# Performance work log

Hardware: AMD Instinct MI355X
Metric: run time of the kernel (lower is better)

The kernel has to match this reference:

```python
import jax, jax.numpy as jnp
import numpy as np
from jax import lax

B, C, H, W = 8, 384, 64, 64


def cos_map(N):
    # ortho DCT-II basis: weight[n, x] = cos(n*(x+0.5)*pi/N) * sqrt(2/N), row 0 /= sqrt(2)
    wx = (jnp.arange(N, dtype=jnp.float32) + 0.5) / N
    wn = jnp.arange(N, dtype=jnp.float32)[:, None]
    w = jnp.cos(wn * wx[None, :] * jnp.pi) * np.sqrt(2.0 / N).astype(np.float32)
    return w.at[0, :].multiply(np.float32(1.0 / np.sqrt(2.0)))


def setup_inputs() -> dict:
    key = jax.random.key(0)
    ks = jax.random.split(key, 8)
    s = 0.05
    return {
        "x": jax.random.normal(ks[0], (B, C, H, W), jnp.float32),
        "freq_embed": jax.random.normal(ks[1], (H, W, C), jnp.float32),
        "dw_w": jax.random.normal(ks[2], (C, 1, 3, 3), jnp.float32) * s,
        "dw_b": jnp.zeros((C,), jnp.float32),
        "lin_w": jax.random.normal(ks[3], (2 * C, C), jnp.float32) * s,
        "lin_b": jnp.zeros((2 * C,), jnp.float32),
        "tok_w": jax.random.normal(ks[4], (C, C), jnp.float32) * s,
        "tok_b": jnp.zeros((C,), jnp.float32),
        "c": jnp.ones((1,), jnp.float32),
        "alpha": jnp.ones((1,), jnp.float32) * 0.1,
        "ln_g": jnp.ones((C,), jnp.float32),
        "ln_b": jnp.zeros((C,), jnp.float32),
        "out_w": jax.random.normal(ks[5], (C, C), jnp.float32) * s,
        "out_b": jnp.zeros((C,), jnp.float32),
    }


def reference(x, freq_embed, dw_w, dw_b, lin_w, lin_b, tok_w, tok_b, c, alpha, ln_g, ln_b, out_w, out_b):
    Bc, Cc, Hc, Wc = x.shape
    # depthwise 3x3 conv
    x = lax.conv_general_dilated(x, dw_w, (1, 1), 'SAME',
                                 feature_group_count=Cc,
                                 dimension_numbers=('NCHW', 'OIHW', 'NCHW'))
    x = x + dw_b[None, :, None, None]
    # linear to 2C (channels-last), split into signal x and gate z
    xz = jnp.einsum('bchw,dc->bhwd', x, lin_w) + lin_b
    xs, z = xz[..., :Cc], xz[..., Cc:]          # [B,H,W,C]
    xs = jnp.transpose(xs, (0, 3, 1, 2))        # [B,C,H,W]
    # 2D ortho DCT-II: D = Wh @ x @ Ww^T
    Wh, Ww = cos_map(Hc), cos_map(Wc)
    Xd = jnp.einsum('nh,bchw,kw->bcnk', Wh, xs, Ww)
    # learned frequency gating: t = ReLU(Linear(freq_embed)), per (H,W,C)
    t = jax.nn.relu(jnp.einsum('hwc,dc->hwd', freq_embed, tok_w) + tok_b)
    ct = jnp.transpose(jnp.cos(c * t), (2, 0, 1))[None]        # [1,C,H,W]
    st = jnp.transpose(jnp.sin(c * t), (2, 0, 1))[None] / c[0]
    # x_u0 == x_v0 == Xd in the original (dct2d applied twice to same x)
    final = ct * Xd + st * (Xd + 0.5 * alpha[0] * Xd)
    # 2D inverse DCT: x = Wh^T @ D @ Ww
    xi = jnp.einsum('nh,bcnk,kw->bchw', Wh, final, Ww)
    # LayerNorm over channels, gate with SiLU(z), output linear
    y = jnp.transpose(xi, (0, 2, 3, 1))          # [B,H,W,C]
    mu = jnp.mean(y, axis=-1, keepdims=True)
    var = jnp.mean((y - mu) ** 2, axis=-1, keepdims=True)
    y = (y - mu) * lax.rsqrt(var + 1e-5) * ln_g + ln_b
    y = y * jax.nn.silu(z)
    y = jnp.einsum('bhwc,dc->bhwd', y, out_w) + out_b
    return jnp.transpose(y, (0, 3, 1, 2))        # [B,C,H,W]
```

## Files before the change

### kernel.cpp

```cpp
#include <hip/hip_runtime.h>

typedef _Float16 h2 __attribute__((ext_vector_type(2)));
typedef _Float16 h4 __attribute__((ext_vector_type(4)));
typedef _Float16 h8 __attribute__((ext_vector_type(8)));
typedef float    f4 __attribute__((ext_vector_type(4)));

#define MFMA32(a,b,c) __builtin_amdgcn_mfma_f32_16x16x32_f16((a),(b),(c),0,0,0)
#define MFMA16(a,b,c) __builtin_amdgcn_mfma_f32_16x16x16f16((a),(b),(c),0,0,0)

#define B_N 8
#define C_N 384
#define P_N 4096
#define PI_F 3.14159265358979323846f

__device__ __forceinline__ h4 to_h4(f4 v) {
  h4 r; r[0]=(_Float16)v[0]; r[1]=(_Float16)v[1]; r[2]=(_Float16)v[2]; r[3]=(_Float16)v[3];
  return r;
}

__device__ __forceinline__ void gl_lds16(const _Float16* g, _Float16* l) {
  __builtin_amdgcn_global_load_lds(
      (const __attribute__((address_space(1))) void*)g,
      (__attribute__((address_space(3))) void*)l, 16, 0, 0);
}

__global__ __launch_bounds__(256) void k_setup(
    const float* __restrict__ lin_w, const float* __restrict__ tok_w,
    const float* __restrict__ out_w, _Float16* __restrict__ lwh,
    _Float16* __restrict__ twh, _Float16* __restrict__ owh,
    _Float16* __restrict__ wmg, _Float16* __restrict__ wmtg) {
  int t = blockIdx.x * 256 + threadIdx.x;
  if (t < 768*384) lwh[t] = (_Float16)lin_w[t];
  if (t < 384*384) { twh[t] = (_Float16)tok_w[t]; owh[t] = (_Float16)out_w[t]; }
  if (t < 4096) {
    int n = t >> 6, h = t & 63;
    float v = cosf((float)n * ((float)h + 0.5f) * (PI_F / 64.0f)) * 0.1767766952966369f;
    if (n == 0) v *= 0.7071067811865476f;
    wmg[n*64 + h]  = (_Float16)v;
    wmtg[h*64 + n] = (_Float16)v;
  }
}

__global__ __launch_bounds__(256) void k_dwconv(
    const float* __restrict__ x, const float* __restrict__ dww,
    const float* __restrict__ dwb, _Float16* __restrict__ xdw) {
  int blk = blockIdx.x;
  int h = blk & 63;
  int rest = blk >> 6;
  int cgi = rest % 6;
  int b = rest / 6;
  int c0 = cgi * 64;
  int t = threadIdx.x;
  int w = t & 63, ci = t >> 6;
  __shared__ _Float16 buf[64 * 68];
  const float* xb = x + (size_t)b * C_N * P_N;
  int wl = (w > 0)  ? w - 1 : 0;
  int wr = (w < 63) ? w + 1 : 63;
  #pragma unroll
  for (int j = 0; j < 8; j++) {
    int lc = ci * 16 + j * 2;
    h2 pr;
    #pragma unroll
    for (int e = 0; e < 2; e++) {
      int c = c0 + lc + e;
      const float* xc = xb + (size_t)c * P_N;
      float k0=dww[c*9+0],k1=dww[c*9+1],k2=dww[c*9+2];
      float k3=dww[c*9+3],k4=dww[c*9+4],k5=dww[c*9+5];
      float k6=dww[c*9+6],k7=dww[c*9+7],k8=dww[c*9+8];
      float top = (h > 0)  ? xc[(h-1)*64 + w] : 0.0f;
      float mid = xc[h*64 + w];
      float bot = (h < 63) ? xc[(h+1)*64 + w] : 0.0f;
      float tl = __shfl(top, wl, 64), tr = __shfl(top, wr, 64);
      float ml = __shfl(mid, wl, 64), mr = __shfl(mid, wr, 64);
      float bl = __shfl(bot, wl, 64), br = __shfl(bot, wr, 64);
      if (w == 0)  { tl = 0.f; ml = 0.f; bl = 0.f; }
      if (w == 63) { tr = 0.f; mr = 0.f; br = 0.f; }
      float acc = dwb[c];
      acc += k0*tl + k1*top + k2*tr;
      acc += k3*ml + k4*mid + k5*mr;
      acc += k6*bl + k7*bot + k8*br;
      pr[e] = (_Float16)acc;
    }
    *(h2*)&buf[w*68 + lc] = pr;
  }
  __syncthreads();
  _Float16* op = xdw + ((size_t)b*P_N + h*64) * C_N + c0;
  #pragma unroll
  for (int i = 0; i < 4; i++) {
    int flat = (t + 256*i) * 4;
    int pix = flat >> 6, cl = flat & 63;
    *(h4*)&op[(size_t)pix*C_N + cl] = *(const h4*)&buf[pix*68 + cl];
  }
}

__global__ __launch_bounds__(256) void k_gate(
    const float* __restrict__ fe, const _Float16* __restrict__ twh,
    const float* __restrict__ tkb, const float* __restrict__ cc,
    const float* __restrict__ aa, _Float16* __restrict__ g) {
  int pt = blockIdx.x & 63, dt = blockIdx.x >> 6;
  int p0 = pt*64, d0 = dt*64;
  int t = threadIdx.x, lane = t & 63, wave = t >> 6;
  int quad = lane >> 4, l15 = lane & 15;
  int wm_ = wave >> 1, wn = wave & 1;
  __shared__ _Float16 la[64*40], lb[64*40];
  int srow = t >> 2, scg = (t & 3) * 8;
  f4 acc[2][2] = {};
  for (int kc = 0; kc < 384; kc += 32) {
    const float* src = fe + (size_t)(p0 + srow)*384 + kc + scg;
    f4 v0 = *(const f4*)src;
    f4 v1 = *(const f4*)(src + 4);
    h8 hv;
    hv[0]=(_Float16)v0[0]; hv[1]=(_Float16)v0[1]; hv[2]=(_Float16)v0[2]; hv[3]=(_Float16)v0[3];
    hv[4]=(_Float16)v1[0]; hv[5]=(_Float16)v1[1]; hv[6]=(_Float16)v1[2]; hv[7]=(_Float16)v1[3];
    *(h8*)&la[srow*40 + scg] = hv;
    *(h8*)&lb[srow*40 + scg] = *(const h8*)&twh[(size_t)(d0 + srow)*384 + kc + scg];
    __syncthreads();
    h8 a0 = *(const h8*)&la[(wm_*32 + l15)*40 + quad*8];
    h8 a1 = *(const h8*)&la[(wm_*32 + 16 + l15)*40 + quad*8];
    h8 b0 = *(const h8*)&lb[(wn*32 + l15)*40 + quad*8];
    h8 b1 = *(const h8*)&lb[(wn*32 + 16 + l15)*40 + quad*8];
    acc[0][0] = MFMA32(a0, b0, acc[0][0]);
    acc[0][1] = MFMA32(a0, b1, acc[0][1]);
    acc[1][0] = MFMA32(a1, b0, acc[1][0]);
    acc[1][1] = MFMA32(a1, b1, acc[1][1]);
    __syncthreads();
  }
  float c0 = cc[0];
  float s1 = (1.0f + 0.5f*aa[0]) / c0;
  #pragma unroll
  for (int i = 0; i < 2; i++)
  #pragma unroll
  for (int j = 0; j < 2; j++) {
    int d  = d0 + wn*32 + j*16 + l15;
    int pl = wm_*32 + i*16 + quad*4;
    float bias = tkb[d];
    h4 hv;
    #pragma unroll
    for (int r = 0; r < 4; r++) {
      float tv = fmaxf(acc[i][j][r] + bias, 0.0f);
      hv[r] = (_Float16)(__cosf(c0*tv) + s1*__sinf(c0*tv));
    }
    *(h4*)&g[(size_t)d*P_N + p0 + pl] = hv;
  }
}

__global__ __launch_bounds__(256) void k_gemm1(
    const _Float16* __restrict__ xdw, const _Float16* __restrict__ lwh,
    const float* __restrict__ lnb, _Float16* __restrict__ xs,
    _Float16* __restrict__ zs) {
  int pt = blockIdx.x & 31;
  int rest = blockIdx.x >> 5;
  int dt = rest % 6, b = rest / 6;
  int p0 = pt * 128, d0 = dt * 128;
  int t = threadIdx.x, lane = t & 63, wave = t >> 6;
  int quad = lane >> 4, l15 = lane & 15;
  int wm = wave >> 1, wn = wave & 1;
  __shared__ _Float16 la[128 * 32];
  __shared__ _Float16 lb[128 * 32];
  int s_row = lane >> 2;
  int s_col = (lane & 3) * 8;
  const _Float16* ga = xdw + ((size_t)b*P_N + p0) * 384 + s_col;
  const _Float16* gb = lwh + (size_t)d0 * 384 + s_col;
  f4 acc[4][4] = {};
  for (int kc = 0; kc < 384; kc += 32) {
    #pragma unroll
    for (int s = 0; s < 2; s++) {
      int seg = wave * 2 + s;
      int row = seg * 16 + s_row;
      gl_lds16(ga + (size_t)row*384 + kc, &la[seg*512 + lane*8]);
      gl_lds16(gb + (size_t)row*384 + kc, &lb[seg*512 + lane*8]);
    }
    __syncthreads();
    h8 af[4], bf[4];
    #pragma unroll
    for (int i = 0; i < 4; i++) {
      af[i] = *(const h8*)&la[(wm*64 + i*16 + l15)*32 + quad*8];
      bf[i] = *(const h8*)&lb[(wn*64 + i*16 + l15)*32 + quad*8];
    }
    #pragma unroll
    for (int i = 0; i < 4; i++)
    #pragma unroll
    for (int j = 0; j < 4; j++)
      acc[i][j] = MFMA32(af[i], bf[j], acc[i][j]);
    __syncthreads();
  }
  bool isz = (d0 >= 384);
  #pragma unroll
  for (int j = 0; j < 4; j++) {
    int d = d0 + wn*64 + j*16 + l15;
    float bias = lnb[d];
    _Float16* dst = isz ? (zs + ((size_t)b*C_N + (d-384)) * P_N)
                        : (xs + ((size_t)b*C_N + d) * P_N);
    #pragma unroll
    for (int i = 0; i < 4; i++) {
      int p = p0 + wm*64 + i*16 + quad*4;
      h4 hv;
      if (isz) {
        #pragma unroll
        for (int r = 0; r < 4; r++) {
          float v = acc[i][j][r] + bias;
          v = v / (1.0f + __expf(-v));
          hv[r] = (_Float16)v;
        }
      } else {
        #pragma unroll
        for (int r = 0; r < 4; r++) hv[r] = (_Float16)(acc[i][j][r] + bias);
      }
      *(h4*)&dst[p] = hv;
    }
  }
}

__global__ __launch_bounds__(256) void k_dct(
    const _Float16* __restrict__ xs, const _Float16* __restrict__ g,
    const _Float16* __restrict__ wmg, const _Float16* __restrict__ wmtg,
    _Float16* __restrict__ xi) {
  int b = blockIdx.x / 96, cg = blockIdx.x % 96;
  int c0 = cg * 4;
  int t = threadIdx.x, wave = t >> 6, lane = t & 63;
  int quad = lane >> 4, l15 = lane & 15;
  __shared__ _Float16 wm_s[64*72];
  __shared__ _Float16 wmt_s[64*72];
  __shared__ _Float16 pb[4][64*72];
  for (int i = t; i < 512; i += 256) {
    int row = i >> 3, col = (i & 7) * 8;
    *(h8*)&wm_s[row*72 + col]  = *(const h8*)&wmg[row*64 + col];
    *(h8*)&wmt_s[row*72 + col] = *(const h8*)&wmtg[row*64 + col];
  }
  const _Float16* xsb = xs + ((size_t)b*C_N + c0) * P_N;
  for (int i = t; i < 2048; i += 256) {
    int pl = i >> 9, idx = i & 511;
    int p = idx * 8, hh = p >> 6, ww = p & 63;
    *(h8*)&pb[pl][hh*72 + ww] = *(const h8*)&xsb[(size_t)pl*P_N + p];
  }
  __syncthreads();
  h8 aS[4][2], bW[4][2];
  #pragma unroll
  for (int I = 0; I < 4; I++)
  #pragma unroll
  for (int kk = 0; kk < 2; kk++) {
    aS[I][kk] = *(const h8*)&pb[wave][(I*16 + l15)*72 + kk*32 + quad*8];
    bW[I][kk] = *(const h8*)&wm_s[(I*16 + l15)*72 + kk*32 + quad*8];
  }
  h4 t1h[4][4];
  #pragma unroll
  for (int I = 0; I < 4; I++)
  #pragma unroll
  for (int J = 0; J < 4; J++) {
    f4 a = {};
    a = MFMA32(aS[I][0], bW[J][0], a);
    a = MFMA32(aS[I][1], bW[J][1], a);
    t1h[I][J] = to_h4(a);
  }
  __syncthreads();
  const _Float16* gb = g + (size_t)c0 * P_N;
  for (int i = t; i < 2048; i += 256) {
    int pl = i >> 9, idx = i & 511;
    int p = idx * 8, hh = p >> 6, ww = p & 63;
    *(h8*)&pb[pl][hh*72 + ww] = *(const h8*)&gb[(size_t)pl*P_N + p];
  }
  __syncthreads();
  f4 t2[4][4] = {};
  #pragma unroll
  for (int I = 0; I < 4; I++)
  #pragma unroll
  for (int K4 = 0; K4 < 4; K4++) {
    h4 af = *(const h4*)&wm_s[(I*16 + l15)*72 + K4*16 + quad*4];
    #pragma unroll
    for (int J = 0; J < 4; J++) t2[I][J] = MFMA16(af, t1h[K4][J], t2[I][J]);
  }
  h4 fh[4][4];
  #pragma unroll
  for (int I = 0; I < 4; I++)
  #pragma unroll
  for (int J = 0; J < 4; J++) {
    int n0 = I*16 + quad*4, k = J*16 + l15;
    h4 r;
    #pragma unroll
    for (int rr = 0; rr < 4; rr++) {
      float gv = (float)pb[wave][(n0+rr)*72 + k];
      r[rr] = (_Float16)(t2[I][J][rr] * gv);
    }
    fh[I][J] = r;
  }
  f4 t3[4][4] = {};
  #pragma unroll
  for (int J = 0; J < 4; J++)
  #pragma unroll
  for (int K4 = 0; K4 < 4; K4++) {
    h4 bf = *(const h4*)&wmt_s[(J*16 + l15)*72 + K4*16 + quad*4];
    #pragma unroll
    for (int I = 0; I < 4; I++) t3[I][J] = MFMA16(fh[K4][I], bf, t3[I][J]);
  }
  h4 t3h[4][4];
  #pragma unroll
  for (int I = 0; I < 4; I++)
  #pragma unroll
  for (int J = 0; J < 4; J++) t3h[I][J] = to_h4(t3[I][J]);
  f4 t4[4][4] = {};
  #pragma unroll
  for (int I = 0; I < 4; I++)
  #pragma unroll
  for (int K4 = 0; K4 < 4; K4++) {
    h4 af = *(const h4*)&wmt_s[(I*16 + l15)*72 + K4*16 + quad*4];
    #pragma unroll
    for (int J = 0; J < 4; J++) t4[I][J] = MFMA16(af, t3h[K4][J], t4[I][J]);
  }
  #pragma unroll
  for (int I = 0; I < 4; I++)
  #pragma unroll
  for (int J = 0; J < 4; J++) {
    int w0 = I*16 + quad*4, hq = J*16 + l15;
    *(h4*)&pb[wave][hq*72 + w0] = to_h4(t4[I][J]);
  }
  __syncthreads();
  _Float16* xib = xi + ((size_t)b*C_N + c0) * P_N;
  for (int i = t; i < 2048; i += 256) {
    int pl = i >> 9, idx = i & 511;
    int p = idx * 8, hh = p >> 6, ww = p & 63;
    *(h8*)&xib[(size_t)pl*P_N + p] = *(const h8*)&pb[pl][hh*72 + ww];
  }
}

__global__ __launch_bounds__(256) void k_ubuild(
    const _Float16* __restrict__ xi, const _Float16* __restrict__ zs,
    const float* __restrict__ lng, const float* __restrict__ lnbv,
    _Float16* __restrict__ u) {
  int b = blockIdx.x >> 6, pt = blockIdx.x & 63;
  int p0 = pt * 64;
  int t = threadIdx.x;
  __shared__ _Float16 ut[64 * 392];
  __shared__ float red[4][64], red2[4][64];
  __shared__ float muL[64], rsL[64];
  int cr = t >> 3;
  int px0 = (t & 7) * 8;
  const _Float16* xib = xi + (size_t)b * C_N * P_N;
  #pragma unroll
  for (int i = 0; i < 12; i++) {
    int c = cr + 32 * i;
    h8 v = *(const h8*)&xib[(size_t)c * P_N + p0 + px0];
    #pragma unroll
    for (int e = 0; e < 8; e++) ut[(px0 + e) * 392 + c] = v[e];
  }
  __syncthreads();
  int px = t & 63, seg = t >> 6;
  float s = 0.f, ss = 0.f;
  #pragma unroll
  for (int j = 0; j < 12; j++) {
    h8 v = *(const h8*)&ut[px * 392 + seg * 96 + j * 8];
    #pragma unroll
    for (int e = 0; e < 8; e++) { float f = (float)v[e]; s += f; ss += f * f; }
  }
  red[seg][px] = s; red2[seg][px] = ss;
  __syncthreads();
  if (t < 64) {
    float st  = red[0][t] + red[1][t] + red[2][t] + red[3][t];
    float sst = red2[0][t] + red2[1][t] + red2[2][t] + red2[3][t];
    float m = st * (1.f/384.f);
    float var = sst * (1.f/384.f) - m * m;
    muL[t] = m; rsL[t] = rsqrtf(var + 1e-5f);
  }
  __syncthreads();
  const _Float16* zb = zs + (size_t)b * C_N * P_N;
  #pragma unroll
  for (int i = 0; i < 12; i++) {
    int c = cr + 32 * i;
    float g = lng[c], bb = lnbv[c];
    h8 zv = *(const h8*)&zb[(size_t)c * P_N + p0 + px0];
    #pragma unroll
    for (int e = 0; e < 8; e++) {
      int p = px0 + e;
      float y = ((float)ut[p * 392 + c] - muL[p]) * rsL[p] * g + bb;
      ut[p * 392 + c] = (_Float16)(y * (float)zv[e]);
    }
  }
  __syncthreads();
  _Float16* ub = u + ((size_t)b * P_N + p0) * C_N;
  #pragma unroll
  for (int i = 0; i < 12; i++) {
    int idx = t + 256 * i;
    int row = idx / 48, ch = idx % 48;
    *(h8*)&ub[(size_t)row * C_N + ch * 8] = *(const h8*)&ut[row * 392 + ch * 8];
  }
}

__global__ __launch_bounds__(256) void k_gemm2(
    const _Float16* __restrict__ u, const _Float16* __restrict__ owh,
    const float* __restrict__ ob, float* __restrict__ out) {
  int pt = blockIdx.x & 31;
  int rest = blockIdx.x >> 5;
  int dt = rest % 3, b = rest / 3;
  int p0 = pt * 128, d0 = dt * 128;
  int t = threadIdx.x, lane = t & 63, wave = t >> 6;
  int quad = lane >> 4, l15 = lane & 15;
  int wm = wave >> 1, wn = wave & 1;
  __shared__ _Float16 la[128 * 32];
  __shared__ _Float16 lb[128 * 32];
  int s_row = lane >> 2;
  int s_col = (lane & 3) * 8;
  const _Float16* ga = u   + ((size_t)b*P_N + p0) * 384 + s_col;
  const _Float16* gb = owh + (size_t)d0 * 384 + s_col;
  f4 acc[4][4] = {};
  for (int kc = 0; kc < 384; kc += 32) {
    #pragma unroll
    for (int s = 0; s < 2; s++) {
      int seg = wave * 2 + s;
      int row = seg * 16 + s_row;
      gl_lds16(ga + (size_t)row*384 + kc, &la[seg*512 + lane*8]);
      gl_lds16(gb + (size_t)row*384 + kc, &lb[seg*512 + lane*8]);
    }
    __syncthreads();
    h8 af[4], bf[4];
    #pragma unroll
    for (int i = 0; i < 4; i++) {
      af[i] = *(const h8*)&la[(wm*64 + i*16 + l15)*32 + quad*8];
      bf[i] = *(const h8*)&lb[(wn*64 + i*16 + l15)*32 + quad*8];
    }
    #pragma unroll
    for (int i = 0; i < 4; i++)
    #pragma unroll
    for (int j = 0; j < 4; j++)
      acc[i][j] = MFMA32(af[i], bf[j], acc[i][j]);
    __syncthreads();
  }
  #pragma unroll
  for (int j = 0; j < 4; j++) {
    int d = d0 + wn*64 + j*16 + l15;
    float bias = ob[d];
    #pragma unroll
    for (int i = 0; i < 4; i++) {
      int p = p0 + wm*64 + i*16 + quad*4;
      f4 v;
      #pragma unroll
      for (int r = 0; r < 4; r++) v[r] = acc[i][j][r] + bias;
      *(f4*)&out[((size_t)b*C_N + d)*P_N + p] = v;
    }
  }
}

extern "C" void kernel_launch(void* const* d_in, const int* in_sizes, int n_in,
                              void* d_out, int out_size, void* d_ws, size_t ws_size,
                              hipStream_t stream) {
  (void)in_sizes; (void)n_in; (void)out_size; (void)ws_size;
  const float* x    = (const float*)d_in[0];
  const float* fe   = (const float*)d_in[1];
  const float* dww  = (const float*)d_in[2];
  const float* dwb  = (const float*)d_in[3];
  const float* linw = (const float*)d_in[4];
  const float* linb = (const float*)d_in[5];
  const float* tokw = (const float*)d_in[6];
  const float* tokb = (const float*)d_in[7];
  const float* cc   = (const float*)d_in[8];
  const float* aa   = (const float*)d_in[9];
  const float* lng  = (const float*)d_in[10];
  const float* lnbv = (const float*)d_in[11];
  const float* outw = (const float*)d_in[12];
  const float* outb = (const float*)d_in[13];
  float* out = (float*)d_out;

  char* ws = (char*)d_ws;
  size_t off = 0;
  auto alloc = [&](size_t bytes) -> void* {
    void* p = ws + off;
    off += (bytes + 255) & ~(size_t)255;
    return p;
  };
  _Float16* lwh  = (_Float16*)alloc((size_t)768*384*2);
  _Float16* twh  = (_Float16*)alloc((size_t)384*384*2);
  _Float16* owh  = (_Float16*)alloc((size_t)384*384*2);
  _Float16* wmg  = (_Float16*)alloc((size_t)64*64*2);
  _Float16* wmtg = (_Float16*)alloc((size_t)64*64*2);
  _Float16* xdw  = (_Float16*)alloc((size_t)B_N*P_N*C_N*2);
  _Float16* xs   = (_Float16*)alloc((size_t)B_N*C_N*P_N*2);
  _Float16* zs   = (_Float16*)alloc((size_t)B_N*C_N*P_N*2);
  _Float16* gg   = (_Float16*)alloc((size_t)C_N*P_N*2);
  _Float16* xi   = xdw;
  _Float16* uu   = xs;

  k_setup<<<1152, 256, 0, stream>>>(linw, tokw, outw, lwh, twh, owh, wmg, wmtg);
  k_dwconv<<<3072, 256, 0, stream>>>(x, dww, dwb, xdw);
  k_gate<<<384, 256, 0, stream>>>(fe, twh, tokb, cc, aa, gg);
  k_gemm1<<<1536, 256, 0, stream>>>(xdw, lwh, linb, xs, zs);
  k_dct<<<768, 256, 0, stream>>>(xs, gg, wmg, wmtg, xi);
  k_ubuild<<<512, 256, 0, stream>>>(xi, zs, lng, lnbv, uu);
  k_gemm2<<<768, 256, 0, stream>>>(uu, owh, outb, out);
}
```

Baseline: 257.9 us.

## Stage full-K weight tile in LDS and stream activations from global in GEMMs

Both pointwise GEMMs switch from 128x128 tiles with per-K-step LDS staging of both operands and two barriers per step, to 128x64 tiles. Each block preloads the whole 64x384 weight slice into padded LDS once, and each wave reads its A fragments straight from global memory. This removes the per-iteration barriers and the LDS round-trip for activations, and doubles the grid size. In exchange, each activation row is now read by twice as many blocks, so global A traffic rises, and the direct global loads are not software-pipelined.

```diff
diff --git a/kernel.cpp b/kernel.cpp
--- a/kernel.cpp
+++ b/kernel.cpp
@@ -16,12 +16,6 @@
 __device__ __forceinline__ h4 to_h4(f4 v) {
   h4 r; r[0]=(_Float16)v[0]; r[1]=(_Float16)v[1]; r[2]=(_Float16)v[2]; r[3]=(_Float16)v[3];
   return r;
-}
-
-__device__ __forceinline__ void gl_lds16(const _Float16* g, _Float16* l) {
-  __builtin_amdgcn_global_load_lds(
-      (const __attribute__((address_space(1))) void*)g,
-      (__attribute__((address_space(3))) void*)l, 16, 0, 0);
 }
 
 __global__ __launch_bounds__(256) void k_setup(
@@ -150,50 +144,45 @@
     _Float16* __restrict__ zs) {
   int pt = blockIdx.x & 31;
   int rest = blockIdx.x >> 5;
-  int dt = rest % 6, b = rest / 6;
-  int p0 = pt * 128, d0 = dt * 128;
+  int dt = rest % 12, b = rest / 12;
+  int p0 = pt * 128, d0 = dt * 64;
   int t = threadIdx.x, lane = t & 63, wave = t >> 6;
   int quad = lane >> 4, l15 = lane & 15;
-  int wm = wave >> 1, wn = wave & 1;
-  __shared__ _Float16 la[128 * 32];
-  __shared__ _Float16 lb[128 * 32];
-  int s_row = lane >> 2;
-  int s_col = (lane & 3) * 8;
-  const _Float16* ga = xdw + ((size_t)b*P_N + p0) * 384 + s_col;
-  const _Float16* gb = lwh + (size_t)d0 * 384 + s_col;
-  f4 acc[4][4] = {};
+  __shared__ _Float16 lbs[64 * 392];
+  {
+    int row = t >> 2, cb = (t & 3) * 8;
+    const _Float16* gB = lwh + (size_t)(d0 + row) * 384;
+    #pragma unroll
+    for (int i = 0; i < 12; i++)
+      *(h8*)&lbs[row*392 + cb + i*32] = *(const h8*)&gB[cb + i*32];
+  }
+  __syncthreads();
+  const _Float16* pa = xdw + ((size_t)b*P_N + p0 + wave*32 + l15) * 384 + quad*8;
+  f4 acc[2][4] = {};
+  #pragma unroll
   for (int kc = 0; kc < 384; kc += 32) {
-    #pragma unroll
-    for (int s = 0; s < 2; s++) {
-      int seg = wave * 2 + s;
-      int row = seg * 16 + s_row;
-      gl_lds16(ga + (size_t)row*384 + kc, &la[seg*512 + lane*8]);
-      gl_lds16(gb + (size_t)row*384 + kc, &lb[seg*512 + lane*8]);
-    }
-    __syncthreads();
-    h8 af[4], bf[4];
-    #pragma unroll
-    for (int i = 0; i < 4; i++) {
-      af[i] = *(const h8*)&la[(wm*64 + i*16 + l15)*32 + quad*8];
-      bf[i] = *(const h8*)&lb[(wn*64 + i*16 + l15)*32 + quad*8];
-    }
-    #pragma unroll
-    for (int i = 0; i < 4; i++)
+    h8 a0 = *(const h8*)(pa + kc);
+    h8 a1 = *(const h8*)(pa + 16*384 + kc);
+    h8 bf[4];
     #pragma unroll
     for (int j = 0; j < 4; j++)
-      acc[i][j] = MFMA32(af[i], bf[j], acc[i][j]);
-    __syncthreads();
+      bf[j] = *(const h8*)&lbs[(j*16 + l15)*392 + kc + quad*8];
+    #pragma unroll
+    for (int j = 0; j < 4; j++) {
+      acc[0][j] = MFMA32(a0, bf[j], acc[0][j]);
+      acc[1][j] = MFMA32(a1, bf[j], acc[1][j]);
+    }
   }
   bool isz = (d0 >= 384);
   #pragma unroll
   for (int j = 0; j < 4; j++) {
-    int d = d0 + wn*64 + j*16 + l15;
+    int d = d0 + j*16 + l15;
     float bias = lnb[d];
     _Float16* dst = isz ? (zs + ((size_t)b*C_N + (d-384)) * P_N)
                         : (xs + ((size_t)b*C_N + d) * P_N);
     #pragma unroll
-    for (int i = 0; i < 4; i++) {
-      int p = p0 + wm*64 + i*16 + quad*4;
+    for (int i = 0; i < 2; i++) {
+      int p = p0 + wave*32 + i*16 + quad*4;
       h4 hv;
       if (isz) {
         #pragma unroll
@@ -389,47 +378,42 @@
     const float* __restrict__ ob, float* __restrict__ out) {
   int pt = blockIdx.x & 31;
   int rest = blockIdx.x >> 5;
-  int dt = rest % 3, b = rest / 3;
-  int p0 = pt * 128, d0 = dt * 128;
+  int dt = rest % 6, b = rest / 6;
+  int p0 = pt * 128, d0 = dt * 64;
   int t = threadIdx.x, lane = t & 63, wave = t >> 6;
   int quad = lane >> 4, l15 = lane & 15;
-  int wm = wave >> 1, wn = wave & 1;
-  __shared__ _Float16 la[128 * 32];
-  __shared__ _Float16 lb[128 * 32];
-  int s_row = lane >> 2;
-  int s_col = (lane & 3) * 8;
-  const _Float16* ga = u   + ((size_t)b*P_N + p0) * 384 + s_col;
-  const _Float16* gb = owh + (size_t)d0 * 384 + s_col;
-  f4 acc[4][4] = {};
+  __shared__ _Float16 lbs[64 * 392];
+  {
+    int row = t >> 2, cb = (t & 3) * 8;
+    const _Float16* gB = owh + (size_t)(d0 + row) * 384;
+    #pragma unroll
+    for (int i = 0; i < 12; i++)
+      *(h8*)&lbs[row*392 + cb + i*32] = *(const h8*)&gB[cb + i*32];
+  }
+  __syncthreads();
+  const _Float16* pa = u + ((size_t)b*P_N + p0 + wave*32 + l15) * 384 + quad*8;
+  f4 acc[2][4] = {};
+  #pragma unroll
   for (int kc = 0; kc < 384; kc += 32) {
-    #pragma unroll
-    for (int s = 0; s < 2; s++) {
-      int seg = wave * 2 + s;
-      int row = seg * 16 + s_row;
-      gl_lds16(ga + (size_t)row*384 + kc, &la[seg*512 + lane*8]);
-      gl_lds16(gb + (size_t)row*384 + kc, &lb[seg*512 + lane*8]);
-    }
-    __syncthreads();
-    h8 af[4], bf[4];
-    #pragma unroll
-    for (int i = 0; i < 4; i++) {
-      af[i] = *(const h8*)&la[(wm*64 + i*16 + l15)*32 + quad*8];
-      bf[i] = *(const h8*)&lb[(wn*64 + i*16 + l15)*32 + quad*8];
-    }
-    #pragma unroll
-    for (int i = 0; i < 4; i++)
+    h8 a0 = *(const h8*)(pa + kc);
+    h8 a1 = *(const h8*)(pa + 16*384 + kc);
+    h8 bf[4];
     #pragma unroll
     for (int j = 0; j < 4; j++)
-      acc[i][j] = MFMA32(af[i], bf[j], acc[i][j]);
-    __syncthreads();
+      bf[j] = *(const h8*)&lbs[(j*16 + l15)*392 + kc + quad*8];
+    #pragma unroll
+    for (int j = 0; j < 4; j++) {
+      acc[0][j] = MFMA32(a0, bf[j], acc[0][j]);
+      acc[1][j] = MFMA32(a1, bf[j], acc[1][j]);
+    }
   }
   #pragma unroll
   for (int j = 0; j < 4; j++) {
-    int d = d0 + wn*64 + j*16 + l15;
+    int d = d0 + j*16 + l15;
     float bias = ob[d];
     #pragma unroll
-    for (int i = 0; i < 4; i++) {
-      int p = p0 + wm*64 + i*16 + quad*4;
+    for (int i = 0; i < 2; i++) {
+      int p = p0 + wave*32 + i*16 + quad*4;
       f4 v;
       #pragma unroll
       for (int r = 0; r < 4; r++) v[r] = acc[i][j][r] + bias;
@@ -480,8 +464,8 @@
   k_setup<<<1152, 256, 0, stream>>>(linw, tokw, outw, lwh, twh, owh, wmg, wmtg);
   k_dwconv<<<3072, 256, 0, stream>>>(x, dww, dwb, xdw);
   k_gate<<<384, 256, 0, stream>>>(fe, twh, tokb, cc, aa, gg);
-  k_gemm1<<<1536, 256, 0, stream>>>(xdw, lwh, linb, xs, zs);
+  k_gemm1<<<3072, 256, 0, stream>>>(xdw, lwh, linb, xs, zs);
   k_dct<<<768, 256, 0, stream>>>(xs, gg, wmg, wmtg, xi);
   k_ubuild<<<512, 256, 0, stream>>>(xi, zs, lng, lnbv, uu);
-  k_gemm2<<<768, 256, 0, stream>>>(uu, owh, outb, out);
-}
+  k_gemm2<<<1536, 256, 0, stream>>>(uu, owh, outb, out);
+}
```

After: 270.7 us. 5.0% more time.
